# Kernel optimization log

Hardware: AMD Instinct MI355X
Metric: run time of the kernel (lower is better)

Reference implementation:

```python
import jax, jax.numpy as jnp
import numpy as np

B, T, E = 4, 2048, 2048
NH, NKV, HD = 16, 4, 128
THETA = 10000.0


def _rope(x, pos_ids, theta):
    # x: [b, h, t, hd]; pos_ids: [b, t]; theta: [hd/2]
    ang = pos_ids[:, None, :, None].astype(jnp.float32) * theta  # [b,1,t,hd/2]
    cos, sin = jnp.cos(ang), jnp.sin(ang)
    x1, x2 = x[..., ::2], x[..., 1::2]
    # interleave rotated pairs back to [..., hd]
    rot = jnp.stack([x1 * cos - x2 * sin, x1 * sin + x2 * cos], axis=-1)
    return rot.reshape(x.shape)


def setup_inputs() -> dict:
    key = jax.random.key(0)
    ks = jax.random.split(key, 10)
    s = 0.02
    x = jax.random.normal(ks[0], (B, T, E), dtype=jnp.float32)
    attention_mask = jax.random.randint(ks[1], (B, T, T), 0, 2, dtype=jnp.int32)
    # torch nn.Linear weights stored here as [in, out] (y = x @ W + b)
    Wq = jax.random.normal(ks[2], (E, E), dtype=jnp.float32) * s
    bq = jnp.zeros((E,), dtype=jnp.float32)
    Wk = jax.random.normal(ks[3], (E, NKV * HD), dtype=jnp.float32) * s
    bk = jnp.zeros((NKV * HD,), dtype=jnp.float32)
    Wv = jax.random.normal(ks[4], (E, NKV * HD), dtype=jnp.float32) * s
    bv = jnp.zeros((NKV * HD,), dtype=jnp.float32)
    Wo = jax.random.normal(ks[5], (E, E), dtype=jnp.float32) * s
    bo = jnp.zeros((E,), dtype=jnp.float32)
    return {"x": x, "attention_mask": attention_mask, "Wq": Wq, "bq": bq,
            "Wk": Wk, "bk": bk, "Wv": Wv, "bv": bv, "Wo": Wo, "bo": bo}


def reference(x, attention_mask, Wq, bq, Wk, bk, Wv, bv, Wo, bo):
    b, t = x.shape[0], x.shape[1]
    # faithful to original: plain reshape (view), NOT transpose-based head split
    q = (x @ Wq + bq).reshape(b, NH, t, HD)
    k = (x @ Wk + bk).reshape(b, NKV, t, HD)
    v = (x @ Wv + bv).reshape(b, NKV, t, HD)
    theta = THETA ** (-jnp.arange(0, HD, 2, dtype=jnp.float32) / HD)
    pos = jnp.broadcast_to(jnp.arange(t), (b, t))
    # original RoPE.forward is wrapped in @torch.no_grad() -> stop_gradient
    k = jax.lax.stop_gradient(_rope(k, pos, theta))
    v = jax.lax.stop_gradient(_rope(v, pos, theta))  # note: RoPE applied to V too
    g = NH // NKV
    k = jnp.tile(k, (1, g, 1, 1))  # torch .repeat tiles kv heads
    v = jnp.tile(v, (1, g, 1, 1))
    # original divides by head_dim ** (-0.5) == multiply by sqrt(head_dim)
    scores = jnp.einsum('bhqd,bhkd->bhqk', q, k) * (HD ** 0.5)
    scores = jnp.where(attention_mask[:, None, :, :] == 0, jnp.float32(1e-9), scores)
    attn = jax.nn.softmax(scores, axis=-1)  # dropout inactive (eval mode)
    out = jnp.einsum('bhqk,bhkd->bhqd', attn, v)
    out = out.transpose(0, 2, 1, 3).reshape(b, t, NH * HD)
    return out @ Wo + bo
```

## Files before the change

### kernel.cpp

```cpp
#include <hip/hip_runtime.h>
#include <math.h>

constexpr int Bc   = 4;
constexpr int Tc   = 2048;
constexpr int Ec   = 2048;
constexpr int NHc  = 16;
constexpr int NKVc = 4;
constexpr int HDc  = 128;
constexpr int KVEc = NKVc * HDc;

typedef __attribute__((ext_vector_type(8))) short bf16x8;
typedef __attribute__((ext_vector_type(4))) short short4v;
typedef __attribute__((ext_vector_type(4))) float f32x4;

__device__ __forceinline__ short f2bf(float f) {
    union { float f; unsigned u; } v; v.f = f;
    unsigned r = v.u + 0x7FFF + ((v.u >> 16) & 1);
    return (short)(r >> 16);
}
__device__ __forceinline__ float bf2f(short s) {
    union { unsigned u; float f; } v; v.u = ((unsigned)(unsigned short)s) << 16;
    return v.f;
}
__device__ __forceinline__ void gload16(const void* g, void* l) {
    __builtin_amdgcn_global_load_lds(
        (const __attribute__((address_space(1))) unsigned*)g,
        (__attribute__((address_space(3))) unsigned*)l, 16, 0, 0);
}

__global__ __launch_bounds__(256)
void convert_split(const float* __restrict__ X, short* __restrict__ Xhi,
                   short* __restrict__ Xlo)
{
    int i = blockIdx.x * 256 + threadIdx.x;
    float4 v = ((const float4*)X)[i];
    float fv[4] = {v.x, v.y, v.z, v.w};
    short4v hi, lo;
    #pragma unroll
    for (int j = 0; j < 4; ++j) {
        hi[j] = f2bf(fv[j]);
        lo[j] = f2bf(fv[j] - bf2f(hi[j]));
    }
    ((short4v*)Xhi)[i] = hi;
    ((short4v*)Xlo)[i] = lo;
}

__global__ __launch_bounds__(256)
void transpose_split(const float* __restrict__ W, short* __restrict__ WThi,
                     short* __restrict__ WTlo, int K, int N)
{
    __shared__ float Ls[32][33];
    const int k0 = blockIdx.x * 32, n0 = blockIdx.y * 32;
    const int t = threadIdx.x;
    const int r = t >> 3, c4 = (t & 7) << 2;
    float4 v = *(const float4*)(W + (size_t)(k0 + r) * N + n0 + c4);
    Ls[r][c4 + 0] = v.x; Ls[r][c4 + 1] = v.y;
    Ls[r][c4 + 2] = v.z; Ls[r][c4 + 3] = v.w;
    __syncthreads();
    short4v hi, lo;
    #pragma unroll
    for (int i = 0; i < 4; ++i) {
        float f = Ls[c4 + i][r];
        hi[i] = f2bf(f);
        lo[i] = f2bf(f - bf2f(hi[i]));
    }
    *(short4v*)(WThi + (size_t)(n0 + r) * K + k0 + c4) = hi;
    if (WTlo) *(short4v*)(WTlo + (size_t)(n0 + r) * K + k0 + c4) = lo;
}

__global__ __launch_bounds__(256)
void mask_bits(const int* __restrict__ mask, unsigned long long* __restrict__ Mb)
{
    const int widx = blockIdx.x * 4 + (threadIdx.x >> 6);
    const int L = threadIdx.x & 63;
    const int m = mask[(size_t)widx * 64 + L];
    unsigned long long bits = __ballot(m != 0);
    if (L == 0) Mb[widx] = bits;
}

template <bool SPLIT>
__global__ __launch_bounds__(256, 2)
void gemm_mfma(const short* __restrict__ Ahi, const short* __restrict__ Alo,
               const short* __restrict__ Bhi, const short* __restrict__ Blo,
               const float* __restrict__ bias, float* __restrict__ C,
               int M, int N, int K)
{
    __shared__ short AsH[128 * 32];
    __shared__ short BsH[128 * 32];
    __shared__ short AsL[SPLIT ? 128 * 32 : 8];
    __shared__ short BsL[SPLIT ? 128 * 32 : 8];

    const int t = threadIdx.x;
    const int w = t >> 6, L = t & 63;
    const int l16 = L & 15, quad = L >> 4;
    const int wr = w >> 1, wc = w & 1;
    const int bm = blockIdx.x * 128, bn = blockIdx.y * 128;

    const int sm = L >> 2;
    const int sq = ((L & 3) - (sm >> 2)) & 3;
    const int scol = sq * 8;

    f32x4 acc[4][4];
    #pragma unroll
    for (int mi = 0; mi < 4; ++mi)
        #pragma unroll
        for (int ni = 0; ni < 4; ++ni) acc[mi][ni] = (f32x4){0, 0, 0, 0};

    const int fxor = (quad + (l16 >> 2)) & 3;

    for (int k0 = 0; k0 < K; k0 += 32) {
        __syncthreads();
        #pragma unroll
        for (int i = 0; i < 2; ++i) {
            const int wl = w * 2 + i;
            const size_t ra = (size_t)(bm + wl * 16 + sm) * K + k0 + scol;
            const size_t rb = (size_t)(bn + wl * 16 + sm) * K + k0 + scol;
            gload16(Ahi + ra, &AsH[wl * 512]);
            gload16(Bhi + rb, &BsH[wl * 512]);
            if (SPLIT) {
                gload16(Alo + ra, &AsL[wl * 512]);
                gload16(Blo + rb, &BsL[wl * 512]);
            }
        }
        __syncthreads();

        bf16x8 ah[4], bh[4], al[4], bl[4];
        #pragma unroll
        for (int mi = 0; mi < 4; ++mi) {
            const int ch = ((wr * 4 + mi) * 64 + l16 * 4 + fxor) * 8;
            ah[mi] = *(const bf16x8*)&AsH[ch];
            if (SPLIT) al[mi] = *(const bf16x8*)&AsL[ch];
        }
        #pragma unroll
        for (int ni = 0; ni < 4; ++ni) {
            const int ch = ((wc * 4 + ni) * 64 + l16 * 4 + fxor) * 8;
            bh[ni] = *(const bf16x8*)&BsH[ch];
            if (SPLIT) bl[ni] = *(const bf16x8*)&BsL[ch];
        }
        #pragma unroll
        for (int mi = 0; mi < 4; ++mi)
            #pragma unroll
            for (int ni = 0; ni < 4; ++ni) {
                acc[mi][ni] = __builtin_amdgcn_mfma_f32_16x16x32_bf16(
                    ah[mi], bh[ni], acc[mi][ni], 0, 0, 0);
                if (SPLIT) {
                    acc[mi][ni] = __builtin_amdgcn_mfma_f32_16x16x32_bf16(
                        al[mi], bh[ni], acc[mi][ni], 0, 0, 0);
                    acc[mi][ni] = __builtin_amdgcn_mfma_f32_16x16x32_bf16(
                        ah[mi], bl[ni], acc[mi][ni], 0, 0, 0);
                }
            }
    }

    #pragma unroll
    for (int ni = 0; ni < 4; ++ni) {
        const int col = bn + wc * 64 + ni * 16 + l16;
        const float bv = bias[col];
        #pragma unroll
        for (int mi = 0; mi < 4; ++mi) {
            #pragma unroll
            for (int r = 0; r < 4; ++r) {
                const int row = bm + wr * 64 + mi * 16 + quad * 4 + r;
                C[(size_t)row * N + col] = acc[mi][ni][r] + bv;
            }
        }
    }
}

__global__ __launch_bounds__(256)
void rope_k(const float* __restrict__ X2d, short* __restrict__ Khi,
            short* __restrict__ Klo)
{
    const int idx = blockIdx.x * 256 + threadIdx.x;
    const int j  = idx & 63;
    const int tk = (idx >> 6) & (Tc - 1);
    const int kh = (idx >> 17) & (NKVc - 1);
    const int bb = idx >> 19;
    const int row = (kh << 9) + (tk >> 2);
    const int col = ((tk & 3) << 7) + (j << 1);
    const float* src = X2d + ((size_t)bb * Tc + row) * KVEc + col;
    const float a = src[0];
    const float b = src[1];
    const float theta = powf(10000.0f, -(float)j * (1.0f / 64.0f));
    const float ang = (float)tk * theta;
    float s, c;
    sincosf(ang, &s, &c);
    const float r0 = a * c - b * s;
    const float r1 = a * s + b * c;
    const size_t off = (((size_t)bb * NKVc + kh) * Tc + tk) * HDc + (j << 1);
    short h0 = f2bf(r0), h1 = f2bf(r1);
    Khi[off]     = h0;  Klo[off]     = f2bf(r0 - bf2f(h0));
    Khi[off + 1] = h1;  Klo[off + 1] = f2bf(r1 - bf2f(h1));
}

__global__ __launch_bounds__(256)
void rope_v_t(const float* __restrict__ V2d, short* __restrict__ Vt)
{
    __shared__ short Ls[128][40];
    const int g  = blockIdx.x;
    const int kh = blockIdx.y;
    const int bb = blockIdx.z;
    const int t  = threadIdx.x;

    const float* src = V2d + ((size_t)bb * Tc + (kh << 9) + (g << 3)) * KVEc;
    #pragma unroll
    for (int i = 0; i < 4; ++i) {
        int e = i * 256 + t;
        float4 v = ((const float4*)src)[e];
        int row = e >> 7;
        int col = (e & 127) << 2;
        int tkl = (row << 2) + (col >> 7);
        int d0  = col & 127;
        int tk  = (g << 5) + tkl;
        float fv[4] = {v.x, v.y, v.z, v.w};
        #pragma unroll
        for (int p = 0; p < 2; ++p) {
            int j = (d0 >> 1) + p;
            float theta = powf(10000.0f, -(float)j * (1.0f / 64.0f));
            float ang = (float)tk * theta;
            float s, c;
            sincosf(ang, &s, &c);
            float a = fv[2 * p], b = fv[2 * p + 1];
            Ls[d0 + 2 * p    ][tkl] = f2bf(a * c - b * s);
            Ls[d0 + 2 * p + 1][tkl] = f2bf(a * s + b * c);
        }
    }
    __syncthreads();
    const int d = t >> 1;
    const int h16 = (t & 1) << 4;
    short* dst = Vt + (((size_t)bb * NKVc + kh) * HDc + d) * Tc + (g << 5) + h16;
    bf16x8 o0 = *(const bf16x8*)&Ls[d][h16];
    bf16x8 o1 = *(const bf16x8*)&Ls[d][h16 + 8];
    *(bf16x8*)dst = o0;
    *(bf16x8*)(dst + 8) = o1;
}

__global__ __launch_bounds__(256, 2)
void attn_mfma(const float* __restrict__ Q2d, const short* __restrict__ Khi_g,
               const short* __restrict__ Klo_g, const short* __restrict__ Vt_g,
               const unsigned long long* __restrict__ Mb, short* __restrict__ AObf)
{
    constexpr int SP = 72;
    __shared__ short KhiS[64 * 128];
    __shared__ short KloS[64 * 128];
    __shared__ short VtS [128 * 64];
    __shared__ short Ps  [64 * SP];

    const int qb = blockIdx.x;
    const int h  = blockIdx.y;
    const int bb = blockIdx.z;
    const int t  = threadIdx.x;
    const int w    = t >> 6;
    const int L    = t & 63;
    const int l16  = L & 15;
    const int quad = L >> 4;
    const int kh   = h & (NKVc - 1);
    const int tq0  = qb * 64 + w * 16;

    bf16x8 qhi[4], qlo[4];
    {
        const float* qrow = Q2d +
            ((size_t)(bb * Tc + h * HDc + qb * 4 + w)) * Ec + 128 * l16;
        #pragma unroll
        for (int kc = 0; kc < 4; ++kc) {
            const float* p = qrow + kc * 32 + quad * 8;
            #pragma unroll
            for (int j = 0; j < 8; ++j) {
                float f = p[j];
                short hi = f2bf(f);
                qhi[kc][j] = hi;
                qlo[kc][j] = f2bf(f - bf2f(hi));
            }
        }
    }

    float m_r[4], lp[4];
    #pragma unroll
    for (int r = 0; r < 4; ++r) { m_r[r] = -INFINITY; lp[r] = 0.0f; }
    f32x4 o[8];
    #pragma unroll
    for (int nc = 0; nc < 8; ++nc) o[nc] = (f32x4){0, 0, 0, 0};

    const short* kbh = Khi_g + ((size_t)(bb * NKVc + kh)) * Tc * HDc;
    const short* kbl = Klo_g + ((size_t)(bb * NKVc + kh)) * Tc * HDc;
    const short* vb  = Vt_g  + ((size_t)(bb * NKVc + kh)) * HDc * Tc;
    const unsigned long long* mrow0 =
        Mb + ((size_t)(bb * Tc + tq0 + quad * 4)) * (Tc / 64);
    const float scale = 11.313708498984761f;

    const int km   = L >> 4;
    const int kpos = L & 15;
    const int vm   = L >> 3;
    const int vc   = ((L & 7) - vm) & 7;

    for (int kt = 0; kt < Tc / 64; ++kt) {
        unsigned long long mw[4];
        #pragma unroll
        for (int r = 0; r < 4; ++r)
            mw[r] = mrow0[(size_t)r * (Tc / 64) + kt];

        __syncthreads();

        #pragma unroll
        for (int i = 0; i < 4; ++i) {
            const int wl = w * 4 + i;
            const int krow = wl * 4 + km;
            const int kc_ = (kpos - (krow & 15)) & 15;
            const size_t go = (size_t)(kt * 64 + krow) * HDc + kc_ * 8;
            gload16(kbh + go, &KhiS[wl * 512]);
            gload16(kbl + go, &KloS[wl * 512]);
            const int vrow = wl * 8 + vm;
            gload16(vb + (size_t)vrow * Tc + kt * 64 + vc * 8, &VtS[wl * 512]);
        }
        __syncthreads();

        f32x4 s[4];
        #pragma unroll
        for (int nt = 0; nt < 4; ++nt) {
            f32x4 acc = (f32x4){0, 0, 0, 0};
            #pragma unroll
            for (int kc = 0; kc < 4; ++kc) {
                const int ch = (((nt * 4 + (l16 >> 2)) << 6) + ((l16 & 3) << 4)
                                + ((kc * 4 + quad + l16) & 15)) << 3;
                bf16x8 khiF = *(const bf16x8*)&KhiS[ch];
                bf16x8 kloF = *(const bf16x8*)&KloS[ch];
                acc = __builtin_amdgcn_mfma_f32_16x16x32_bf16(qhi[kc], khiF, acc, 0, 0, 0);
                acc = __builtin_amdgcn_mfma_f32_16x16x32_bf16(qlo[kc], khiF, acc, 0, 0, 0);
                acc = __builtin_amdgcn_mfma_f32_16x16x32_bf16(qhi[kc], kloF, acc, 0, 0, 0);
            }
            s[nt] = acc;
        }

        #pragma unroll
        for (int r = 0; r < 4; ++r) {
            const unsigned t0 = (unsigned)(mw[r] >> l16);
            const unsigned t1 = (unsigned)(mw[r] >> (l16 + 32));
            s[0][r] = (t0 & 1u)       ? s[0][r] * scale : 1e-9f;
            s[1][r] = (t0 & 0x10000u) ? s[1][r] * scale : 1e-9f;
            s[2][r] = (t1 & 1u)       ? s[2][r] * scale : 1e-9f;
            s[3][r] = (t1 & 0x10000u) ? s[3][r] * scale : 1e-9f;
        }

        float mt[4];
        #pragma unroll
        for (int r = 0; r < 4; ++r)
            mt[r] = fmaxf(fmaxf(s[0][r], s[1][r]), fmaxf(s[2][r], s[3][r]));
        #pragma unroll
        for (int off = 1; off < 16; off <<= 1)
            #pragma unroll
            for (int r = 0; r < 4; ++r)
                mt[r] = fmaxf(mt[r], __shfl_xor(mt[r], off));

        float al[4];
        bool need = false;
        #pragma unroll
        for (int r = 0; r < 4; ++r) {
            const float mn = fmaxf(m_r[r], mt[r]);
            al[r] = __expf(m_r[r] - mn);
            need |= (al[r] < 1.0f);
            m_r[r] = mn;
        }

        float rsum[4];
        #pragma unroll
        for (int r = 0; r < 4; ++r) {
            float p0 = __expf(s[0][r] - m_r[r]);
            float p1 = __expf(s[1][r] - m_r[r]);
            float p2 = __expf(s[2][r] - m_r[r]);
            float p3 = __expf(s[3][r] - m_r[r]);
            s[0][r] = p0; s[1][r] = p1; s[2][r] = p2; s[3][r] = p3;
            rsum[r] = (p0 + p1) + (p2 + p3);
        }

        if (__any(need)) {
            #pragma unroll
            for (int r = 0; r < 4; ++r) lp[r] *= al[r];
            #pragma unroll
            for (int nc = 0; nc < 8; ++nc)
                #pragma unroll
                for (int r = 0; r < 4; ++r)
                    o[nc][r] *= al[r];
        }
        #pragma unroll
        for (int r = 0; r < 4; ++r) lp[r] += rsum[r];

        #pragma unroll
        for (int nt = 0; nt < 4; ++nt)
            #pragma unroll
            for (int r = 0; r < 4; ++r)
                Ps[(w * 16 + quad * 4 + r) * SP + nt * 16 + l16] = f2bf(s[nt][r]);

        bf16x8 a0 = *(const bf16x8*)&Ps[(w * 16 + l16) * SP + quad * 8];
        bf16x8 a1 = *(const bf16x8*)&Ps[(w * 16 + l16) * SP + 32 + quad * 8];

        #pragma unroll
        for (int nc = 0; nc < 8; ++nc) {
            const int rg = (nc * 2 + (l16 >> 3)) << 6;
            const int rm = l16 & 7;
            const int ch0 = (rg + (rm << 3) + ((quad + rm) & 7)) << 3;
            const int ch1 = (rg + (rm << 3) + ((quad + 4 + rm) & 7)) << 3;
            bf16x8 b0 = *(const bf16x8*)&VtS[ch0];
            bf16x8 b1 = *(const bf16x8*)&VtS[ch1];
            o[nc] = __builtin_amdgcn_mfma_f32_16x16x32_bf16(a0, b0, o[nc], 0, 0, 0);
            o[nc] = __builtin_amdgcn_mfma_f32_16x16x32_bf16(a1, b1, o[nc], 0, 0, 0);
        }
    }

    #pragma unroll
    for (int off = 1; off < 16; off <<= 1)
        #pragma unroll
        for (int r = 0; r < 4; ++r)
            lp[r] += __shfl_xor(lp[r], off);

    float inv[4];
    #pragma unroll
    for (int r = 0; r < 4; ++r) inv[r] = 1.0f / lp[r];
    #pragma unroll
    for (int r = 0; r < 4; ++r) {
        short* orow = AObf + ((size_t)(bb * Tc + tq0 + quad * 4 + r)) * Ec
                           + h * HDc + l16;
        #pragma unroll
        for (int nc = 0; nc < 8; ++nc)
            orow[nc * 16] = f2bf(o[nc][r] * inv[r]);
    }
}

extern "C" void kernel_launch(void* const* d_in, const int* in_sizes, int n_in,
                              void* d_out, int out_size, void* d_ws, size_t ws_size,
                              hipStream_t stream)
{
    const float* x    = (const float*)d_in[0];
    const int*  amask = (const int*)  d_in[1];
    const float* Wq   = (const float*)d_in[2];
    const float* bq   = (const float*)d_in[3];
    const float* Wk   = (const float*)d_in[4];
    const float* bk   = (const float*)d_in[5];
    const float* Wv   = (const float*)d_in[6];
    const float* bv   = (const float*)d_in[7];
    const float* Wo   = (const float*)d_in[8];
    const float* bo   = (const float*)d_in[9];
    float* out = (float*)d_out;

    char* ws = (char*)d_ws;
    float* Q2d   = (float*)(ws);
    short* Xhi   = (short*)(ws + 67108864);
    short* Xlo   = (short*)(ws + 100663296);
    short* WqThi = (short*)(ws + 134217728);
    short* WqTlo = (short*)(ws + 134217728 + 8388608);
    float* K2d   = (float*)(ws + 150994944);
    float* V2d   = (float*)(ws + 100663296);
    short* Khi   = (short*)(ws + 100663296 + 16777216);
    short* Klo   = (short*)(ws + 100663296 + 25165824);
    short* WkThi = (short*)(ws + 134217728);
    short* WkTlo = (short*)(ws + 134217728 + 2097152);
    short* WvThi = (short*)(ws + 134217728 + 4194304);
    short* WoThi = (short*)(ws + 134217728 + 8388608);
    short* Vt    = (short*)(ws + 150994944);
    short* AObf  = (short*)(ws + 67108864);
    unsigned long long* Mb = (unsigned long long*)(ws + 167772160);

    const int M = Bc * Tc;
    dim3 blk(256);

    mask_bits<<<(Bc * Tc * (Tc / 64)) / 4, blk, 0, stream>>>(amask, Mb);
    transpose_split<<<dim3(Ec / 32, Ec / 32), blk, 0, stream>>>(Wq, WqThi, WqTlo, Ec, Ec);
    convert_split<<<(M * Ec / 4) / 256, blk, 0, stream>>>(x, Xhi, Xlo);
    gemm_mfma<true><<<dim3(M / 128, Ec / 128), blk, 0, stream>>>(
        Xhi, Xlo, WqThi, WqTlo, bq, Q2d, M, Ec, Ec);
    transpose_split<<<dim3(Ec / 32, KVEc / 32), blk, 0, stream>>>(Wk, WkThi, WkTlo, Ec, KVEc);
    transpose_split<<<dim3(Ec / 32, KVEc / 32), blk, 0, stream>>>(Wv, WvThi, nullptr, Ec, KVEc);
    transpose_split<<<dim3(Ec / 32, Ec / 32), blk, 0, stream>>>(Wo, WoThi, nullptr, Ec, Ec);
    gemm_mfma<true><<<dim3(M / 128, KVEc / 128), blk, 0, stream>>>(
        Xhi, Xlo, WkThi, WkTlo, bk, K2d, M, KVEc, Ec);
    gemm_mfma<false><<<dim3(M / 128, KVEc / 128), blk, 0, stream>>>(
        Xhi, nullptr, WvThi, nullptr, bv, V2d, M, KVEc, Ec);
    rope_k<<<(Bc * NKVc * Tc * 64) / 256, blk, 0, stream>>>(K2d, Khi, Klo);
    rope_v_t<<<dim3(Tc / 32, NKVc, Bc), blk, 0, stream>>>(V2d, Vt);
    attn_mfma<<<dim3(Tc / 64, NHc, Bc), blk, 0, stream>>>(
        Q2d, Khi, Klo, Vt, Mb, AObf);
    gemm_mfma<false><<<dim3(M / 128, Ec / 128), blk, 0, stream>>>(
        AObf, nullptr, WoThi, nullptr, bo, out, M, Ec, Ec);
}
```

Baseline: 1.083 ms.

## Process two query tiles per warp in attention and fold softmax scale into Wq

The attention kernel now handles 128 queries per block, 32 per warp, as two 16-row groups. Each K/V tile loaded into LDS is reused across twice as many query rows, halving the number of K/V tile loads and block launches. The sqrt(hd)*log2(e) scale is folded into the Wq weights and bias, so the softmax uses a raw exp2 with no per-score multiply, and the masked value becomes 1e-9*log2(e). The cost is about twice the accumulator and Q-fragment registers per warp, which may lower occupancy under the launch bound of 2, plus a larger P buffer in LDS.

```diff
diff --git a/kernel.cpp b/kernel.cpp
--- a/kernel.cpp
+++ b/kernel.cpp
@@ -22,6 +22,11 @@
     union { unsigned u; float f; } v; v.u = ((unsigned)(unsigned short)s) << 16;
     return v.f;
 }
+#if __has_builtin(__builtin_amdgcn_exp2f)
+__device__ __forceinline__ float ex2(float x) { return __builtin_amdgcn_exp2f(x); }
+#else
+__device__ __forceinline__ float ex2(float x) { return exp2f(x); }
+#endif
 __device__ __forceinline__ void gload16(const void* g, void* l) {
     __builtin_amdgcn_global_load_lds(
         (const __attribute__((address_space(1))) unsigned*)g,
@@ -47,7 +52,7 @@
 
 __global__ __launch_bounds__(256)
 void transpose_split(const float* __restrict__ W, short* __restrict__ WThi,
-                     short* __restrict__ WTlo, int K, int N)
+                     short* __restrict__ WTlo, int K, int N, float scale)
 {
     __shared__ float Ls[32][33];
     const int k0 = blockIdx.x * 32, n0 = blockIdx.y * 32;
@@ -60,7 +65,7 @@
     short4v hi, lo;
     #pragma unroll
     for (int i = 0; i < 4; ++i) {
-        float f = Ls[c4 + i][r];
+        float f = Ls[c4 + i][r] * scale;
         hi[i] = f2bf(f);
         lo[i] = f2bf(f - bf2f(hi[i]));
     }
@@ -83,7 +88,7 @@
 void gemm_mfma(const short* __restrict__ Ahi, const short* __restrict__ Alo,
                const short* __restrict__ Bhi, const short* __restrict__ Blo,
                const float* __restrict__ bias, float* __restrict__ C,
-               int M, int N, int K)
+               int M, int N, int K, float bscale)
 {
     __shared__ short AsH[128 * 32];
     __shared__ short BsH[128 * 32];
@@ -155,7 +160,7 @@
     #pragma unroll
     for (int ni = 0; ni < 4; ++ni) {
         const int col = bn + wc * 64 + ni * 16 + l16;
-        const float bv = bias[col];
+        const float bv = bias[col] * bscale;
         #pragma unroll
         for (int mi = 0; mi < 4; ++mi) {
             #pragma unroll
@@ -244,7 +249,7 @@
     __shared__ short KhiS[64 * 128];
     __shared__ short KloS[64 * 128];
     __shared__ short VtS [128 * 64];
-    __shared__ short Ps  [64 * SP];
+    __shared__ short Ps  [128 * SP];
 
     const int qb = blockIdx.x;
     const int h  = blockIdx.y;
@@ -255,12 +260,15 @@
     const int l16  = L & 15;
     const int quad = L >> 4;
     const int kh   = h & (NKVc - 1);
-    const int tq0  = qb * 64 + w * 16;
-
-    bf16x8 qhi[4], qlo[4];
-    {
+    const int tq0  = qb * 128 + w * 32;
+
+    const float MASKED = 1.4426950408889634e-9f;
+
+    bf16x8 qhi[2][4], qlo[2][4];
+    #pragma unroll
+    for (int g = 0; g < 2; ++g) {
         const float* qrow = Q2d +
-            ((size_t)(bb * Tc + h * HDc + qb * 4 + w)) * Ec + 128 * l16;
+            ((size_t)(bb * Tc + h * HDc + qb * 8 + w * 2 + g)) * Ec + 128 * l16;
         #pragma unroll
         for (int kc = 0; kc < 4; ++kc) {
             const float* p = qrow + kc * 32 + quad * 8;
@@ -268,25 +276,28 @@
             for (int j = 0; j < 8; ++j) {
                 float f = p[j];
                 short hi = f2bf(f);
-                qhi[kc][j] = hi;
-                qlo[kc][j] = f2bf(f - bf2f(hi));
-            }
-        }
-    }
-
-    float m_r[4], lp[4];
-    #pragma unroll
-    for (int r = 0; r < 4; ++r) { m_r[r] = -INFINITY; lp[r] = 0.0f; }
-    f32x4 o[8];
-    #pragma unroll
-    for (int nc = 0; nc < 8; ++nc) o[nc] = (f32x4){0, 0, 0, 0};
+                qhi[g][kc][j] = hi;
+                qlo[g][kc][j] = f2bf(f - bf2f(hi));
+            }
+        }
+    }
+
+    float m_r[2][4], lp[2][4];
+    #pragma unroll
+    for (int g = 0; g < 2; ++g)
+        #pragma unroll
+        for (int r = 0; r < 4; ++r) { m_r[g][r] = -INFINITY; lp[g][r] = 0.0f; }
+    f32x4 o[2][8];
+    #pragma unroll
+    for (int g = 0; g < 2; ++g)
+        #pragma unroll
+        for (int nc = 0; nc < 8; ++nc) o[g][nc] = (f32x4){0, 0, 0, 0};
 
     const short* kbh = Khi_g + ((size_t)(bb * NKVc + kh)) * Tc * HDc;
     const short* kbl = Klo_g + ((size_t)(bb * NKVc + kh)) * Tc * HDc;
     const short* vb  = Vt_g  + ((size_t)(bb * NKVc + kh)) * HDc * Tc;
     const unsigned long long* mrow0 =
         Mb + ((size_t)(bb * Tc + tq0 + quad * 4)) * (Tc / 64);
-    const float scale = 11.313708498984761f;
 
     const int km   = L >> 4;
     const int kpos = L & 15;
@@ -294,11 +305,6 @@
     const int vc   = ((L & 7) - vm) & 7;
 
     for (int kt = 0; kt < Tc / 64; ++kt) {
-        unsigned long long mw[4];
-        #pragma unroll
-        for (int r = 0; r < 4; ++r)
-            mw[r] = mrow0[(size_t)r * (Tc / 64) + kt];
-
         __syncthreads();
 
         #pragma unroll
@@ -314,84 +320,104 @@
         }
         __syncthreads();
 
-        f32x4 s[4];
+        f32x4 s[2][4];
         #pragma unroll
         for (int nt = 0; nt < 4; ++nt) {
-            f32x4 acc = (f32x4){0, 0, 0, 0};
+            f32x4 a0 = (f32x4){0, 0, 0, 0};
+            f32x4 a1 = (f32x4){0, 0, 0, 0};
             #pragma unroll
             for (int kc = 0; kc < 4; ++kc) {
                 const int ch = (((nt * 4 + (l16 >> 2)) << 6) + ((l16 & 3) << 4)
                                 + ((kc * 4 + quad + l16) & 15)) << 3;
                 bf16x8 khiF = *(const bf16x8*)&KhiS[ch];
                 bf16x8 kloF = *(const bf16x8*)&KloS[ch];
-                acc = __builtin_amdgcn_mfma_f32_16x16x32_bf16(qhi[kc], khiF, acc, 0, 0, 0);
-                acc = __builtin_amdgcn_mfma_f32_16x16x32_bf16(qlo[kc], khiF, acc, 0, 0, 0);
-                acc = __builtin_amdgcn_mfma_f32_16x16x32_bf16(qhi[kc], kloF, acc, 0, 0, 0);
-            }
-            s[nt] = acc;
-        }
-
-        #pragma unroll
-        for (int r = 0; r < 4; ++r) {
-            const unsigned t0 = (unsigned)(mw[r] >> l16);
-            const unsigned t1 = (unsigned)(mw[r] >> (l16 + 32));
-            s[0][r] = (t0 & 1u)       ? s[0][r] * scale : 1e-9f;
-            s[1][r] = (t0 & 0x10000u) ? s[1][r] * scale : 1e-9f;
-            s[2][r] = (t1 & 1u)       ? s[2][r] * scale : 1e-9f;
-            s[3][r] = (t1 & 0x10000u) ? s[3][r] * scale : 1e-9f;
-        }
-
-        float mt[4];
-        #pragma unroll
-        for (int r = 0; r < 4; ++r)
-            mt[r] = fmaxf(fmaxf(s[0][r], s[1][r]), fmaxf(s[2][r], s[3][r]));
-        #pragma unroll
-        for (int off = 1; off < 16; off <<= 1)
+                a0 = __builtin_amdgcn_mfma_f32_16x16x32_bf16(qhi[0][kc], khiF, a0, 0, 0, 0);
+                a1 = __builtin_amdgcn_mfma_f32_16x16x32_bf16(qhi[1][kc], khiF, a1, 0, 0, 0);
+                a0 = __builtin_amdgcn_mfma_f32_16x16x32_bf16(qlo[0][kc], khiF, a0, 0, 0, 0);
+                a1 = __builtin_amdgcn_mfma_f32_16x16x32_bf16(qlo[1][kc], khiF, a1, 0, 0, 0);
+                a0 = __builtin_amdgcn_mfma_f32_16x16x32_bf16(qhi[0][kc], kloF, a0, 0, 0, 0);
+                a1 = __builtin_amdgcn_mfma_f32_16x16x32_bf16(qhi[1][kc], kloF, a1, 0, 0, 0);
+            }
+            s[0][nt] = a0;
+            s[1][nt] = a1;
+        }
+
+        #pragma unroll
+        for (int g = 0; g < 2; ++g) {
+            unsigned long long mw[4];
             #pragma unroll
             for (int r = 0; r < 4; ++r)
-                mt[r] = fmaxf(mt[r], __shfl_xor(mt[r], off));
-
-        float al[4];
-        bool need = false;
-        #pragma unroll
-        for (int r = 0; r < 4; ++r) {
-            const float mn = fmaxf(m_r[r], mt[r]);
-            al[r] = __expf(m_r[r] - mn);
-            need |= (al[r] < 1.0f);
-            m_r[r] = mn;
-        }
-
-        float rsum[4];
-        #pragma unroll
-        for (int r = 0; r < 4; ++r) {
-            float p0 = __expf(s[0][r] - m_r[r]);
-            float p1 = __expf(s[1][r] - m_r[r]);
-            float p2 = __expf(s[2][r] - m_r[r]);
-            float p3 = __expf(s[3][r] - m_r[r]);
-            s[0][r] = p0; s[1][r] = p1; s[2][r] = p2; s[3][r] = p3;
-            rsum[r] = (p0 + p1) + (p2 + p3);
-        }
-
-        if (__any(need)) {
-            #pragma unroll
-            for (int r = 0; r < 4; ++r) lp[r] *= al[r];
-            #pragma unroll
-            for (int nc = 0; nc < 8; ++nc)
+                mw[r] = mrow0[(size_t)(g * 16 + r) * (Tc / 64) + kt];
+
+            #pragma unroll
+            for (int r = 0; r < 4; ++r) {
+                const unsigned t0 = (unsigned)(mw[r] >> l16);
+                const unsigned t1 = (unsigned)(mw[r] >> (l16 + 32));
+                s[g][0][r] = (t0 & 1u)       ? s[g][0][r] : MASKED;
+                s[g][1][r] = (t0 & 0x10000u) ? s[g][1][r] : MASKED;
+                s[g][2][r] = (t1 & 1u)       ? s[g][2][r] : MASKED;
+                s[g][3][r] = (t1 & 0x10000u) ? s[g][3][r] : MASKED;
+            }
+
+            float mt[4];
+            #pragma unroll
+            for (int r = 0; r < 4; ++r)
+                mt[r] = fmaxf(fmaxf(s[g][0][r], s[g][1][r]),
+                              fmaxf(s[g][2][r], s[g][3][r]));
+            #pragma unroll
+            for (int off = 1; off < 16; off <<= 1)
                 #pragma unroll
                 for (int r = 0; r < 4; ++r)
-                    o[nc][r] *= al[r];
-        }
-        #pragma unroll
-        for (int r = 0; r < 4; ++r) lp[r] += rsum[r];
-
-        #pragma unroll
-        for (int nt = 0; nt < 4; ++nt)
-            #pragma unroll
-            for (int r = 0; r < 4; ++r)
-                Ps[(w * 16 + quad * 4 + r) * SP + nt * 16 + l16] = f2bf(s[nt][r]);
-
-        bf16x8 a0 = *(const bf16x8*)&Ps[(w * 16 + l16) * SP + quad * 8];
-        bf16x8 a1 = *(const bf16x8*)&Ps[(w * 16 + l16) * SP + 32 + quad * 8];
+                    mt[r] = fmaxf(mt[r], __shfl_xor(mt[r], off));
+
+            float al[4];
+            bool need = false;
+            #pragma unroll
+            for (int r = 0; r < 4; ++r) {
+                need |= (mt[r] > m_r[g][r]);
+                const float mn = fmaxf(m_r[g][r], mt[r]);
+                al[r] = ex2(m_r[g][r] - mn);
+                m_r[g][r] = mn;
+            }
+
+            float rsum[4];
+            #pragma unroll
+            for (int r = 0; r < 4; ++r) {
+                float p0 = ex2(s[g][0][r] - m_r[g][r]);
+                float p1 = ex2(s[g][1][r] - m_r[g][r]);
+                float p2 = ex2(s[g][2][r] - m_r[g][r]);
+                float p3 = ex2(s[g][3][r] - m_r[g][r]);
+                s[g][0][r] = p0; s[g][1][r] = p1;
+                s[g][2][r] = p2; s[g][3][r] = p3;
+                rsum[r] = (p0 + p1) + (p2 + p3);
+            }
+
+            if (__any(need)) {
+                #pragma unroll
+                for (int r = 0; r < 4; ++r) lp[g][r] *= al[r];
+                #pragma unroll
+                for (int nc = 0; nc < 8; ++nc)
+                    #pragma unroll
+                    for (int r = 0; r < 4; ++r)
+                        o[g][nc][r] *= al[r];
+            }
+            #pragma unroll
+            for (int r = 0; r < 4; ++r) lp[g][r] += rsum[r];
+
+            #pragma unroll
+            for (int nt = 0; nt < 4; ++nt)
+                #pragma unroll
+                for (int r = 0; r < 4; ++r)
+                    Ps[(w * 32 + g * 16 + quad * 4 + r) * SP + nt * 16 + l16]
+                        = f2bf(s[g][nt][r]);
+        }
+
+        bf16x8 pa[2][2];
+        #pragma unroll
+        for (int g = 0; g < 2; ++g) {
+            pa[g][0] = *(const bf16x8*)&Ps[(w * 32 + g * 16 + l16) * SP + quad * 8];
+            pa[g][1] = *(const bf16x8*)&Ps[(w * 32 + g * 16 + l16) * SP + 32 + quad * 8];
+        }
 
         #pragma unroll
         for (int nc = 0; nc < 8; ++nc) {
@@ -401,27 +427,32 @@
             const int ch1 = (rg + (rm << 3) + ((quad + 4 + rm) & 7)) << 3;
             bf16x8 b0 = *(const bf16x8*)&VtS[ch0];
             bf16x8 b1 = *(const bf16x8*)&VtS[ch1];
-            o[nc] = __builtin_amdgcn_mfma_f32_16x16x32_bf16(a0, b0, o[nc], 0, 0, 0);
-            o[nc] = __builtin_amdgcn_mfma_f32_16x16x32_bf16(a1, b1, o[nc], 0, 0, 0);
-        }
-    }
-
-    #pragma unroll
-    for (int off = 1; off < 16; off <<= 1)
-        #pragma unroll
-        for (int r = 0; r < 4; ++r)
-            lp[r] += __shfl_xor(lp[r], off);
-
-    float inv[4];
-    #pragma unroll
-    for (int r = 0; r < 4; ++r) inv[r] = 1.0f / lp[r];
-    #pragma unroll
-    for (int r = 0; r < 4; ++r) {
-        short* orow = AObf + ((size_t)(bb * Tc + tq0 + quad * 4 + r)) * Ec
-                           + h * HDc + l16;
-        #pragma unroll
-        for (int nc = 0; nc < 8; ++nc)
-            orow[nc * 16] = f2bf(o[nc][r] * inv[r]);
+            o[0][nc] = __builtin_amdgcn_mfma_f32_16x16x32_bf16(pa[0][0], b0, o[0][nc], 0, 0, 0);
+            o[1][nc] = __builtin_amdgcn_mfma_f32_16x16x32_bf16(pa[1][0], b0, o[1][nc], 0, 0, 0);
+            o[0][nc] = __builtin_amdgcn_mfma_f32_16x16x32_bf16(pa[0][1], b1, o[0][nc], 0, 0, 0);
+            o[1][nc] = __builtin_amdgcn_mfma_f32_16x16x32_bf16(pa[1][1], b1, o[1][nc], 0, 0, 0);
+        }
+    }
+
+    #pragma unroll
+    for (int g = 0; g < 2; ++g) {
+        #pragma unroll
+        for (int off = 1; off < 16; off <<= 1)
+            #pragma unroll
+            for (int r = 0; r < 4; ++r)
+                lp[g][r] += __shfl_xor(lp[g][r], off);
+        float inv[4];
+        #pragma unroll
+        for (int r = 0; r < 4; ++r) inv[r] = 1.0f / lp[g][r];
+        #pragma unroll
+        for (int r = 0; r < 4; ++r) {
+            short* orow = AObf +
+                ((size_t)(bb * Tc + tq0 + g * 16 + quad * 4 + r)) * Ec
+                + h * HDc + l16;
+            #pragma unroll
+            for (int nc = 0; nc < 8; ++nc)
+                orow[nc * 16] = f2bf(o[g][nc][r] * inv[r]);
+        }
     }
 }
 
@@ -440,6 +471,8 @@
     const float* Wo   = (const float*)d_in[8];
     const float* bo   = (const float*)d_in[9];
     float* out = (float*)d_out;
+
+    const float ALPHA = (float)(11.313708498984761 * 1.4426950408889634);
 
     char* ws = (char*)d_ws;
     float* Q2d   = (float*)(ws);
@@ -463,21 +496,21 @@
     dim3 blk(256);
 
     mask_bits<<<(Bc * Tc * (Tc / 64)) / 4, blk, 0, stream>>>(amask, Mb);
-    transpose_split<<<dim3(Ec / 32, Ec / 32), blk, 0, stream>>>(Wq, WqThi, WqTlo, Ec, Ec);
+    transpose_split<<<dim3(Ec / 32, Ec / 32), blk, 0, stream>>>(Wq, WqThi, WqTlo, Ec, Ec, ALPHA);
     convert_split<<<(M * Ec / 4) / 256, blk, 0, stream>>>(x, Xhi, Xlo);
     gemm_mfma<true><<<dim3(M / 128, Ec / 128), blk, 0, stream>>>(
-        Xhi, Xlo, WqThi, WqTlo, bq, Q2d, M, Ec, Ec);
-    transpose_split<<<dim3(Ec / 32, KVEc / 32), blk, 0, stream>>>(Wk, WkThi, WkTlo, Ec, KVEc);
-    transpose_split<<<dim3(Ec / 32, KVEc / 32), blk, 0, stream>>>(Wv, WvThi, nullptr, Ec, KVEc);
-    transpose_split<<<dim3(Ec / 32, Ec / 32), blk, 0, stream>>>(Wo, WoThi, nullptr, Ec, Ec);
+        Xhi, Xlo, WqThi, WqTlo, bq, Q2d, M, Ec, Ec, ALPHA);
+    transpose_split<<<dim3(Ec / 32, KVEc / 32), blk, 0, stream>>>(Wk, WkThi, WkTlo, Ec, KVEc, 1.0f);
+    transpose_split<<<dim3(Ec / 32, KVEc / 32), blk, 0, stream>>>(Wv, WvThi, nullptr, Ec, KVEc, 1.0f);
+    transpose_split<<<dim3(Ec / 32, Ec / 32), blk, 0, stream>>>(Wo, WoThi, nullptr, Ec, Ec, 1.0f);
     gemm_mfma<true><<<dim3(M / 128, KVEc / 128), blk, 0, stream>>>(
-        Xhi, Xlo, WkThi, WkTlo, bk, K2d, M, KVEc, Ec);
+        Xhi, Xlo, WkThi, WkTlo, bk, K2d, M, KVEc, Ec, 1.0f);
     gemm_mfma<false><<<dim3(M / 128, KVEc / 128), blk, 0, stream>>>(
-        Xhi, nullptr, WvThi, nullptr, bv, V2d, M, KVEc, Ec);
+        Xhi, nullptr, WvThi, nullptr, bv, V2d, M, KVEc, Ec, 1.0f);
     rope_k<<<(Bc * NKVc * Tc * 64) / 256, blk, 0, stream>>>(K2d, Khi, Klo);
     rope_v_t<<<dim3(Tc / 32, NKVc, Bc), blk, 0, stream>>>(V2d, Vt);
-    attn_mfma<<<dim3(Tc / 64, NHc, Bc), blk, 0, stream>>>(
+    attn_mfma<<<dim3(Tc / 128, NHc, Bc), blk, 0, stream>>>(
         Q2d, Khi, Klo, Vt, Mb, AObf);
     gemm_mfma<false><<<dim3(M / 128, Ec / 128), blk, 0, stream>>>(
-        AObf, nullptr, WoThi, nullptr, bo, out, M, Ec, Ec);
-}
+        AObf, nullptr, WoThi, nullptr, bo, out, M, Ec, Ec, 1.0f);
+}
```

Result: slower. 1.192 ms (+10.1%).
